# Optimization experiments

Hardware: AMD Instinct MI355X
Metric: run time of the kernel (lower is better)

Reference implementation:

```python
import jax, jax.numpy as jnp
import numpy as np

K = 15  # PSF kernel size


def conv3(x, w, b):
    # 3x3 conv, stride 1, padding 1, NCHW/OIHW
    y = jax.lax.conv_general_dilated(x, w, (1, 1), ((1, 1), (1, 1)),
                                     dimension_numbers=("NCHW", "OIHW", "NCHW"))
    return y + b[None, :, None, None]


def setup_inputs() -> dict:
    key = jax.random.key(0)
    ks = jax.random.split(key, 22)
    S = 0.05  # small init scale to keep activations / softmax logits sane
    p = lambda k, shape: (jax.random.normal(k, shape, jnp.float32) * S)
    return {
        "raw_image": jax.random.uniform(ks[0], (1, 4, 256, 256), jnp.float32),
        "aberration_features": jax.random.normal(ks[1], (1, 128, 256, 256), jnp.float32),
        # psf_predictor: 128->256->128->4*225
        "pw1": p(ks[2], (256, 128, 3, 3)), "pb1": p(ks[3], (256,)),
        "pw2": p(ks[4], (128, 256, 3, 3)), "pb2": p(ks[5], (128,)),
        "pw3": p(ks[6], (900, 128, 3, 3)), "pb3": p(ks[7], (900,)),
        # freq_corrector: 8->64->64->8
        "fw1": p(ks[8], (64, 8, 3, 3)),  "fb1": p(ks[9], (64,)),
        "fw2": p(ks[10], (64, 64, 3, 3)), "fb2": p(ks[11], (64,)),
        "fw3": p(ks[12], (8, 64, 3, 3)),  "fb3": p(ks[13], (8,)),
        # per-channel correctors (4 of them), stacked on leading dim: 1->16->16->1
        "cw1": p(ks[14], (4, 16, 1, 3, 3)),  "cb1": p(ks[15], (4, 16)),
        "cw2": p(ks[16], (4, 16, 16, 3, 3)), "cb2": p(ks[17], (4, 16)),
        "cw3": p(ks[18], (4, 1, 16, 3, 3)),  "cb3": p(ks[19], (4, 1)),
    }


def reference(raw_image, aberration_features,
              pw1, pb1, pw2, pb2, pw3, pb3,
              fw1, fb1, fw2, fb2, fw3, fb3,
              cw1, cb1, cw2, cb2, cw3, cb3):
    B, C, H, W = raw_image.shape
    # --- PSF prediction ---
    h = jax.nn.relu(conv3(aberration_features, pw1, pb1))
    h = jax.nn.relu(conv3(h, pw2, pb2))
    psf = conv3(h, pw3, pb3).reshape(B, C, K * K, H, W)
    psf = jax.nn.softmax(psf, axis=2)  # normalize over the K*K taps
    # --- spatially-varying deconv: unfold + weighted reduce ---
    pad = K // 2
    xp = jnp.pad(raw_image, ((0, 0), (0, 0), (pad, pad), (pad, pad)), mode="reflect")
    patches = jax.lax.conv_general_dilated_patches(
        xp, (K, K), (1, 1), "VALID", dimension_numbers=("NCHW", "OIHW", "NCHW"))
    patches = patches.reshape(B, C, K * K, H, W)  # channel-major like F.unfold
    corrected = jnp.sum(patches * psf, axis=2)  # [B,C,H,W]
    # --- frequency-domain correction ---
    fft = jnp.fft.rfft2(corrected, norm="ortho")  # [B,C,H,W//2+1] complex
    fri = jnp.concatenate([fft.real, fft.imag], axis=1)  # [B,2C,...]
    g = jax.nn.relu(conv3(fri, fw1, fb1))
    g = jax.nn.relu(conv3(g, fw2, fb2))
    g = conv3(g, fw3, fb3)
    cf = jax.lax.complex(g[:, :C], g[:, C:])
    corrected = corrected + jnp.fft.irfft2(cf, s=(H, W), norm="ortho")
    # --- per-channel refinement (4 small distinct conv stacks) ---
    outs = []
    for i in range(C):
        ch = corrected[:, i:i + 1]
        ch = jax.nn.relu(conv3(ch, cw1[i], cb1[i]))
        ch = jax.nn.relu(conv3(ch, cw2[i], cb2[i]))
        ch = conv3(ch, cw3[i], cb3[i])
        outs.append(ch)
    corrected = jnp.concatenate(outs, axis=1)
    return jnp.clip(raw_image + corrected, 0.0, 1.0)
```

## Files before the change

### kernel.cpp

```cpp
#include <hip/hip_runtime.h>
#include <hip/hip_bf16.h>
#include <math.h>

#define PI_F 3.14159265358979323846f
#define PERM4(s) ((((s)&3)) + 8*(((s)>>2)&1) + 4*((s)>>3))

typedef short bfrag __attribute__((ext_vector_type(8)));
typedef float f32x4 __attribute__((ext_vector_type(4)));
typedef float f32x16 __attribute__((ext_vector_type(16)));
typedef unsigned short us8 __attribute__((ext_vector_type(8)));

__device__ inline unsigned bf16rne(float x) {
    unsigned u = __builtin_bit_cast(unsigned, x);
    return (u + 0x7fffu + ((u >> 16) & 1u)) >> 16;
}
__device__ inline unsigned packbf2(float a, float b) {
    return bf16rne(a) | (bf16rne(b) << 16);
}
__device__ inline float bf2f(unsigned short u) {
    return __builtin_bit_cast(float, (unsigned)u << 16);
}
__device__ inline void glds16(const unsigned short* g, unsigned char* l) {
    __builtin_amdgcn_global_load_lds(
        (const __attribute__((address_space(1))) unsigned int*)g,
        (__attribute__((address_space(3))) unsigned int*)l, 16, 0, 0);
}

template<bool RELU, int CT, bool SM>
__global__ __launch_bounds__(256, (CT == 2) ? 4 : 5) void conv_v9(
    const unsigned short* __restrict__ inb, const short* __restrict__ wp,
    const float* __restrict__ bias, unsigned short* __restrict__ ob,
    int C32, int Cout, int COT, int CBmax,
    const float* __restrict__ rawc, float* __restrict__ corr)
{
    int bid = blockIdx.x;
    bid = (bid & 7) * 128 + (bid >> 3);
    const int y  = bid >> 2;
    const int x0 = (bid & 3) << 6;
    const int t  = threadIdx.x;
    const int l  = t & 63;
    const int col = l & 31, kh = l >> 5;
    const int wv = t >> 6;
    const int ctg0 = wv * CT;

    __shared__ __align__(16) unsigned char sB[2][13824];

    f32x16 acc[CT][2];
#pragma unroll
    for (int ct = 0; ct < CT; ++ct)
#pragma unroll
        for (int n = 0; n < 2; ++n)
#pragma unroll
            for (int i = 0; i < 16; ++i) acc[ct][n][i] = 0.f;

    int ba3[3];
#pragma unroll
    for (int dx = 0; dx < 3; ++dx) {
        int px = col + 3 + dx;
        ba3[dx] = px * 64 + ((kh ^ ((px >> 1) & 3)) << 4);
    }

    int srcoff[4];
    bool vmask[4];
#pragma unroll
    for (int i = 0; i < 4; ++i) {
        int q = i * 256 + t;
        bool qv = q < 864;
        int row = q / 288;  if (row > 2) row = 2;
        int qr = q - row * 288;
        int px = qr >> 2, j = qr & 3;
        int u = j ^ ((px >> 1) & 3);
        int gx = x0 - 4 + px;
        int gy = y - 1 + row;
        vmask[i] = qv && ((unsigned)gx < 256u) && ((unsigned)gy < 256u);
        srcoff[i] = (((u >> 1) * 256 + gy) * 256 + gx) * 16 + (u & 1) * 8;
    }

    auto STAGE = [&](int c32, unsigned char* bufb) {
        const int coff = c32 * 2097152;
#pragma unroll
        for (int i = 0; i < 4; ++i)
            if (vmask[i])
                glds16(inb + (srcoff[i] + coff), bufb + (i << 12) + (wv << 10));
    };

    for (int i = t; i < 1728; i += 256)
        *(uint4*)(&sB[0][0] + i * 16) = make_uint4(0, 0, 0, 0);
    __syncthreads();

    const bfrag* wA = (const bfrag*)wp;
    const int tstr = C32 * 2 * COT * 64;

    auto LOAD_AF = [&](bfrag (&af)[3][CT], int abase, int dy) {
#pragma unroll
        for (int dx = 0; dx < 3; ++dx)
#pragma unroll
            for (int ct = 0; ct < CT; ++ct)
                af[dx][ct] = wA[abase + ct * 64 + (size_t)(dy * 3 + dx) * tstr];
    };
    auto MFMA_DY = [&](const bfrag (&af)[3][CT], const unsigned char* rp, int csx) {
#pragma unroll
        for (int dx = 0; dx < 3; ++dx) {
            const int ba = ba3[dx] ^ csx;
            bfrag b0 = *(const bfrag*)(rp + ba);
            bfrag b1 = *(const bfrag*)(rp + ba + 2048);
#pragma unroll
            for (int ct = 0; ct < CT; ++ct) {
                acc[ct][0] = __builtin_amdgcn_mfma_f32_32x32x16_bf16(af[dx][ct], b0, acc[ct][0], 0, 0, 0);
                acc[ct][1] = __builtin_amdgcn_mfma_f32_32x32x16_bf16(af[dx][ct], b1, acc[ct][1], 0, 0, 0);
            }
        }
    };

    STAGE(0, sB[0]);
    __syncthreads();
    for (int c32 = 0; c32 < C32; ++c32) {
        const unsigned char* bufp = sB[c32 & 1];
        const int ab0 = (c32 * 2 * COT + ctg0) * 64 + l;
        const int ab1 = ((c32 * 2 + 1) * COT + ctg0) * 64 + l;
        bfrag af0[3][CT];
        LOAD_AF(af0, ab0, 0);
        if (c32 + 1 < C32) STAGE(c32 + 1, sB[(c32 + 1) & 1]);
        MFMA_DY(af0, bufp, 0);
#pragma unroll
        for (int dy = 1; dy < 3; ++dy) {
            bfrag af[3][CT];
            LOAD_AF(af, ab0, dy);
            MFMA_DY(af, bufp + dy * 4608, 0);
        }
#pragma unroll
        for (int dy = 0; dy < 3; ++dy) {
            bfrag af[3][CT];
            LOAD_AF(af, ab1, dy);
            MFMA_DY(af, bufp + dy * 4608, 32);
        }
        __syncthreads();
    }

    if (SM) {
        float* sRaw  = (float*)&sB[0][0];
        float* sBias = (float*)&sB[0][4800];
        float* red   = (float*)&sB[1][0];
        for (int i = t; i < 1200; i += 256) {
            int r = i / 80, xx = i - r * 80;
            int gy = y + r - 7;
            gy = gy < 0 ? -gy : (gy > 255 ? 510 - gy : gy);
            int gx = x0 + xx - 7;
            gx = gx < 0 ? -gx : (gx > 255 ? 510 - gx : gx);
            sRaw[i] = rawc[gy * 256 + gx];
        }
        if (t < 225) sBias[t] = bias[t];
        __syncthreads();

        float pm[2], ps[2], pa[2];
#pragma unroll
        for (int n = 0; n < 2; ++n) {
            float m = -1e30f, s = 0.f, a = 0.f;
            const int xb = col + n * 32;
#pragma unroll
            for (int ct = 0; ct < CT; ++ct) {
                const f32x16 A = acc[ct][n];
#pragma unroll
                for (int rh = 0; rh < 2; ++rh) {
                    int cb = (ctg0 + ct) * 2 + rh;
#pragma unroll
                    for (int j = 0; j < 8; ++j) {
                        int co = cb * 16 + (j & 3) + 8 * (j >> 2) + 4 * kh;
                        if (co < 225) {
                            float lv = A[rh * 8 + j] + sBias[co];
                            int ty = co / 15, tx = co - ty * 15;
                            float pv = sRaw[ty * 80 + xb + tx];
                            if (lv > m + 4.f) { float rs = __expf(m - lv); s *= rs; a *= rs; m = lv; }
                            float e = __expf(lv - m);
                            s += e; a += e * pv;
                        }
                    }
                }
            }
            pm[n] = m; ps[n] = s; pa[n] = a;
        }
        const int g = wv * 2 + kh;
#pragma unroll
        for (int n = 0; n < 2; ++n) {
            int px = col + n * 32;
            red[(px * 8 + g) * 3 + 0] = pm[n];
            red[(px * 8 + g) * 3 + 1] = ps[n];
            red[(px * 8 + g) * 3 + 2] = pa[n];
        }
        __syncthreads();
        if (t < 64) {
            float m = red[(t * 8) * 3], s = red[(t * 8) * 3 + 1], a = red[(t * 8) * 3 + 2];
#pragma unroll
            for (int gg = 1; gg < 8; ++gg) {
                float mg = red[(t * 8 + gg) * 3], sg = red[(t * 8 + gg) * 3 + 1], ag = red[(t * 8 + gg) * 3 + 2];
                float M = fmaxf(m, mg);
                float s0 = __expf(m - M), s1 = __expf(mg - M);
                s = s * s0 + sg * s1;
                a = a * s0 + ag * s1;
                m = M;
            }
            corr[y * 256 + x0 + t] = a / s;
        }
    } else {
#pragma unroll
        for (int ct = 0; ct < CT; ++ct) {
            const int ctg = ctg0 + ct;
#pragma unroll
            for (int n = 0; n < 2; ++n) {
                const int xx = x0 + col + n * 32;
                const f32x16 A = acc[ct][n];
#pragma unroll
                for (int rh = 0; rh < 2; ++rh) {
                    int cb = ctg * 2 + rh;
                    if (cb >= CBmax) continue;
                    unsigned wd[4];
#pragma unroll
                    for (int jp = 0; jp < 4; ++jp) {
                        float vv[2];
#pragma unroll
                        for (int e = 0; e < 2; ++e) {
                            int j = jp * 2 + e;
                            int co = cb * 16 + (j & 3) + 8 * (j >> 2) + 4 * kh;
                            float bv = (co < Cout) ? bias[co] : 0.f;
                            float v = A[rh * 8 + j] + bv;
                            if (RELU) v = fmaxf(v, 0.f);
                            vv[e] = v;
                        }
                        wd[jp] = packbf2(vv[0], vv[1]);
                    }
                    *(uint4*)(ob + ((((size_t)cb << 8) + y) * 256 + xx) * 16 + (kh << 3)) =
                        make_uint4(wd[0], wd[1], wd[2], wd[3]);
                }
            }
        }
    }
}

template<bool RELU, bool OUT_BF16, int CT>
__global__ __launch_bounds__(256, 3) void conv_v4(
    const unsigned short* __restrict__ inb, const short* __restrict__ wp,
    const float* __restrict__ bias, void* __restrict__ outv,
    int C32, int Cout, int COT, int W, int RSg, int CBmax)
{
    const int tilesx = (W + 127) >> 7;
    const int y  = blockIdx.x / tilesx;
    const int x0 = (blockIdx.x % tilesx) << 7;
    const int t  = threadIdx.x;
    const int l  = t & 63;
    const int col = l & 31, kh = l >> 5;
    const int wv = t >> 6;
    const int wct = wv & 1, wpt = wv >> 1;
    const int ctg0 = (blockIdx.y * 2 + wct) * CT;

    __shared__ __align__(16) unsigned char sB[26112];

    f32x16 acc[CT][2];
#pragma unroll
    for (int ct = 0; ct < CT; ++ct)
#pragma unroll
        for (int n = 0; n < 2; ++n)
#pragma unroll
            for (int i = 0; i < 16; ++i) acc[ct][n][i] = 0.f;

    int ba3[3];
#pragma unroll
    for (int dx = 0; dx < 3; ++dx) {
        int px = wpt * 64 + col + 3 + dx;
        ba3[dx] = px * 64 + ((kh ^ ((px >> 1) & 3)) << 4);
    }

    const int pxm = (t & 127) + 4, thalf = t >> 7;
    const int gxm = x0 + (t & 127);
    const bool gxok = gxm < W;
    const int offm_e = pxm * 64 + ((thalf ^ ((pxm >> 1) & 3)) << 4);
    const int hr = t >> 5, hj = t & 31, hg = hj >> 3, hp = hj & 7;
    const int hslot = hp + ((hp >> 2) << 7);
    const int hgx = x0 - 4 + hslot;
    const int hoff = hr * 8704 + hslot * 64 + ((hg ^ ((hslot >> 1) & 3)) << 4);
    const int hgy = y + hr - 1;
    const bool hok = (t < 96) && ((unsigned)hgy < 256u) && ((unsigned)hgx < (unsigned)W);

    auto STAGE = [&](int c32) {
        const int cb0 = c32 << 1;
#pragma unroll
        for (int k = 0; k < 6; ++k) {
            const int r = k >> 1;
            const int cb = cb0 + (k & 1);
            const int gy = y + r - 1;
            uint4 v = make_uint4(0, 0, 0, 0);
            if (gxok && (unsigned)gy < 256u)
                v = *(const uint4*)(inb + ((((size_t)cb << 8) + gy) * RSg + gxm) * 16 + (thalf << 3));
            *(uint4*)(sB + r * 8704 + (offm_e ^ ((k & 1) << 5))) = v;
        }
        if (t < 96) {
            uint4 v = make_uint4(0, 0, 0, 0);
            if (hok) v = *(const uint4*)(inb + ((((size_t)(cb0 + (hg >> 1)) << 8) + hgy) * RSg + hgx) * 16 + ((hg & 1) << 3));
            *(uint4*)(sB + hoff) = v;
        }
    };

    const bfrag* wA = (const bfrag*)wp;
    const int tstr = C32 * 2 * COT * 64;

    STAGE(0);
    __syncthreads();
    for (int c32 = 0; c32 < C32; ++c32) {
#pragma unroll 1
        for (int cs = 0; cs < 2; ++cs) {
            const int abase = ((c32 * 2 + cs) * COT + ctg0) * 64 + l;
            const int csx = cs << 5;
#pragma unroll
            for (int dy = 0; dy < 3; ++dy) {
                bfrag af[3][CT];
#pragma unroll
                for (int dx = 0; dx < 3; ++dx)
#pragma unroll
                    for (int ct = 0; ct < CT; ++ct)
                        af[dx][ct] = wA[abase + ct * 64 + (size_t)(dy * 3 + dx) * tstr];
                const unsigned char* rp = sB + dy * 8704;
#pragma unroll
                for (int dx = 0; dx < 3; ++dx) {
                    const int ba = ba3[dx] ^ csx;
                    bfrag b0 = *(const bfrag*)(rp + ba);
                    bfrag b1 = *(const bfrag*)(rp + ba + 2048);
#pragma unroll
                    for (int ct = 0; ct < CT; ++ct) {
                        acc[ct][0] = __builtin_amdgcn_mfma_f32_32x32x16_bf16(af[dx][ct], b0, acc[ct][0], 0, 0, 0);
                        acc[ct][1] = __builtin_amdgcn_mfma_f32_32x32x16_bf16(af[dx][ct], b1, acc[ct][1], 0, 0, 0);
                    }
                }
            }
        }
        __syncthreads();
        if (c32 + 1 < C32) { STAGE(c32 + 1); __syncthreads(); }
    }

    const int xBase = x0 + wpt * 64 + col;
#pragma unroll
    for (int ct = 0; ct < CT; ++ct) {
        const int ctg = ctg0 + ct;
#pragma unroll
        for (int n = 0; n < 2; ++n) {
            int xx = xBase + n * 32;
            if (xx >= W) continue;
            const f32x16 A = acc[ct][n];
            if (OUT_BF16) {
                unsigned short* ob = (unsigned short*)outv;
#pragma unroll
                for (int rh = 0; rh < 2; ++rh) {
                    int cb = ctg * 2 + rh;
                    if (cb >= CBmax) continue;
                    unsigned wd[4];
#pragma unroll
                    for (int jp = 0; jp < 4; ++jp) {
                        float vv[2];
#pragma unroll
                        for (int e = 0; e < 2; ++e) {
                            int j = jp * 2 + e;
                            int co = cb * 16 + (j & 3) + 8 * (j >> 2) + 4 * kh;
                            float bv = (co < Cout) ? bias[co] : 0.f;
                            float v = A[rh * 8 + j] + bv;
                            if (RELU) v = fmaxf(v, 0.f);
                            vv[e] = v;
                        }
                        wd[jp] = packbf2(vv[0], vv[1]);
                    }
                    *(uint4*)(ob + ((((size_t)cb << 8) + y) * RSg + xx) * 16 + (kh << 3)) =
                        make_uint4(wd[0], wd[1], wd[2], wd[3]);
                }
            } else {
                float* of = (float*)outv;
#pragma unroll
                for (int reg = 0; reg < 16; ++reg) {
                    int co = ctg * 32 + (reg & 3) + 8 * (reg >> 2) + 4 * kh;
                    if (co < Cout) {
                        float v = A[reg] + bias[co];
                        if (RELU) v = fmaxf(v, 0.f);
                        of[(((size_t)co << 8) + y) * RSg + xx] = v;
                    }
                }
            }
        }
    }
}

__global__ __launch_bounds__(256) void repack_wA(
    const float* __restrict__ w, unsigned short* __restrict__ o,
    int Cin, int C32, int Cout, int COT)
{
    int total = 9 * C32 * 2 * COT * 512;
    for (int i = blockIdx.x * 256 + threadIdx.x; i < total; i += gridDim.x * 256) {
        int j = i & 7;
        int l = (i >> 3) & 63;
        int rest = i >> 9;
        int ct = rest % COT; rest /= COT;
        int cs = rest & 1; rest >>= 1;
        int c32 = rest % C32;
        int tap = rest / C32;
        int co = ct * 32 + (l & 31);
        int s = ((l >> 5) << 3) + j;
        int ci = c32 * 32 + cs * 16 + PERM4(s);
        float v = (co < Cout && ci < Cin) ? w[((size_t)co * Cin + ci) * 9 + tap] : 0.f;
        o[i] = (unsigned short)bf16rne(v);
    }
}

__global__ __launch_bounds__(256) void cvt_blocked(
    const float* __restrict__ src, unsigned short* __restrict__ dst, int C)
{
    int cb = blockIdx.x >> 8;
    int y  = blockIdx.x & 255;
    int x  = threadIdx.x;
    unsigned wd[8];
#pragma unroll
    for (int q = 0; q < 8; ++q) {
        float v[2];
#pragma unroll
        for (int e = 0; e < 2; ++e) {
            int s = q * 2 + e;
            int ci = (cb << 4) + PERM4(s);
            v[e] = (ci < C) ? src[((size_t)ci * 256 + y) * 256 + x] : 0.f;
        }
        wd[q] = packbf2(v[0], v[1]);
    }
    unsigned short* dp = dst + (((size_t)cb << 16) + (y << 8) + x) * 16;
    *(uint4*)dp = make_uint4(wd[0], wd[1], wd[2], wd[3]);
    *(uint4*)(dp + 8) = make_uint4(wd[4], wd[5], wd[6], wd[7]);
}

__global__ __launch_bounds__(256) void repack_wr2(
    const float* __restrict__ cw2, unsigned short* __restrict__ o)
{
    int i = blockIdx.x * 256 + threadIdx.x;
    if (i >= 10240) return;
    int k = i & 31, rest = i >> 5;
    int co = rest & 15;
    int kt = (rest >> 4) % 5;
    int ch = rest / 80;
    int tap = 2 * kt + (k >= 16 ? 1 : 0), ci = k & 15;
    float v = 0.f;
    if (tap < 9) v = cw2[(((size_t)ch * 16 + co) * 16 + ci) * 9 + tap];
    o[i] = (unsigned short)bf16rne(v);
}

__global__ __launch_bounds__(256) void refine1_kernel(
    const float* __restrict__ corrected, const float* __restrict__ cw1,
    const float* __restrict__ cb1, unsigned short* __restrict__ h1b)
{
    const int c = blockIdx.x >> 8;
    const int y = blockIdx.x & 255;
    const int t = threadIdx.x;
    __shared__ float sIn[3][258];
    __shared__ float sW[144];
    __shared__ float sBv[16];
    if (t < 144) sW[t] = cw1[c * 144 + t];
    if (t >= 144 && t < 160) sBv[t - 144] = cb1[c * 16 + (t - 144)];
    for (int i = t; i < 774; i += 256) {
        int r = i / 258, xx = i % 258;
        int gy = y + r - 1, gx = xx - 1;
        sIn[r][xx] = ((unsigned)gy < 256u && (unsigned)gx < 256u)
                   ? corrected[((size_t)c * 256 + gy) * 256 + gx] : 0.f;
    }
    __syncthreads();
    float a[9];
#pragma unroll
    for (int dy = 0; dy < 3; ++dy)
#pragma unroll
        for (int dx = 0; dx < 3; ++dx) a[dy * 3 + dx] = sIn[dy][t + dx];
    unsigned short ov[16];
#pragma unroll
    for (int co = 0; co < 16; ++co) {
        float acc = sBv[co];
#pragma unroll
        for (int tap = 0; tap < 9; ++tap) acc += a[tap] * sW[co * 9 + tap];
        acc = fmaxf(acc, 0.f);
        ov[co] = (unsigned short)bf16rne(acc);
    }
    unsigned short* op = h1b + ((((size_t)c * 256 + y) * 256 + t) << 4);
    *(uint4*)op = *(uint4*)ov;
    *(uint4*)(op + 8) = *(uint4*)(ov + 8);
}

__global__ __launch_bounds__(256) void refine2_mfma(
    const unsigned short* __restrict__ h1b, const unsigned short* __restrict__ wr2,
    const float* __restrict__ cb2, unsigned short* __restrict__ h2b)
{
    const int c = blockIdx.x >> 8;
    const int y = blockIdx.x & 255;
    const int t = threadIdx.x;
    const int l15 = t & 15, lg = (t >> 4) & 3, wv = t >> 6;

    __shared__ __align__(16) unsigned char sA[3 * 258 * 32];

    for (int i = t; i < 1548; i += 256) {
        int r = i / 516, u = i % 516;
        int px = u >> 1, half = u & 1;
        int gy = y + r - 1, gx = px - 1;
        uint4 v = make_uint4(0, 0, 0, 0);
        if ((unsigned)gy < 256u && (unsigned)gx < 256u)
            v = *(const uint4*)(h1b + ((((size_t)c * 256 + gy) * 256 + gx) << 4) + (half << 3));
        *(uint4*)(sA + r * 8256 + px * 32 + ((half ^ ((px >> 2) & 1)) << 4)) = v;
    }
    __syncthreads();

    f32x4 acc[4];
#pragma unroll
    for (int n = 0; n < 4; ++n) acc[n] = (f32x4){0.f, 0.f, 0.f, 0.f};
    const bfrag* wf = (const bfrag*)(wr2 + (size_t)c * 2560);
    const int strip = wv * 64;
#pragma unroll
    for (int kt = 0; kt < 5; ++kt) {
        bfrag a = wf[(kt * 16 + l15) * 4 + lg];
        int tap1 = 2 * kt + 1; if (tap1 > 8) tap1 = 8;
        int tap = (lg < 2) ? (2 * kt) : tap1;
        int dy = tap / 3, dx = tap % 3;
#pragma unroll
        for (int n = 0; n < 4; ++n) {
            int pxs = strip + n * 16 + l15 + dx;
            bfrag b = *(const bfrag*)(sA + dy * 8256 + pxs * 32 +
                                      (((lg & 1) ^ ((pxs >> 2) & 1)) << 4));
            acc[n] = __builtin_amdgcn_mfma_f32_16x16x32_bf16(a, b, acc[n], 0, 0, 0);
        }
    }

#pragma unroll
    for (int n = 0; n < 4; ++n) {
        int px = strip + n * 16 + l15;
        unsigned short ov[4];
#pragma unroll
        for (int r = 0; r < 4; ++r) {
            int co = lg * 4 + r;
            float v = acc[n][r] + cb2[c * 16 + co];
            v = fmaxf(v, 0.f);
            ov[r] = (unsigned short)bf16rne(v);
        }
        *(ushort4*)(h2b + ((((size_t)c * 256 + y) * 256 + px) << 4) + lg * 4) = *(ushort4*)ov;
    }
}

__global__ __launch_bounds__(256) void refine3_kernel(
    const unsigned short* __restrict__ h2b, const float* __restrict__ cw3,
    const float* __restrict__ cb3, const float* __restrict__ raw,
    float* __restrict__ out)
{
    const int c = blockIdx.x >> 8;
    const int y = blockIdx.x & 255;
    const int t = threadIdx.x;
    __shared__ __align__(16) unsigned char sA[3 * 258 * 32];
    __shared__ float sW[144];
    if (t < 144) sW[t] = cw3[c * 144 + t];
    for (int i = t; i < 1548; i += 256) {
        int r = i / 516, u = i % 516;
        int px = u >> 1, half = u & 1;
        int gy = y + r - 1, gx = px - 1;
        uint4 v = make_uint4(0, 0, 0, 0);
        if ((unsigned)gy < 256u && (unsigned)gx < 256u)
            v = *(const uint4*)(h2b + ((((size_t)c * 256 + gy) * 256 + gx) << 4) + (half << 3));
        *(uint4*)(sA + r * 8256 + px * 32 + ((half ^ ((px >> 2) & 1)) << 4)) = v;
    }
    __syncthreads();
    float acc = cb3[c];
#pragma unroll
    for (int tap = 0; tap < 9; ++tap) {
        int dy = tap / 3, dx = tap % 3;
        int px = t + dx;
        const unsigned char* p = sA + dy * 8256 + px * 32;
        int sw = ((px >> 2) & 1) << 4;
        us8 h0 = *(const us8*)(p + (sw ^ 0));
        us8 h1 = *(const us8*)(p + (sw ^ 16));
#pragma unroll
        for (int j = 0; j < 8; ++j) acc += bf2f(h0[j]) * sW[j * 9 + tap];
#pragma unroll
        for (int j = 0; j < 8; ++j) acc += bf2f(h1[j]) * sW[(8 + j) * 9 + tap];
    }
    size_t idx = ((size_t)c * 256 + y) * 256 + t;
    float v = raw[idx] + acc;
    out[idx] = fminf(fmaxf(v, 0.f), 1.f);
}

__global__ __launch_bounds__(256) void rdft_row_kernel(
    const float* __restrict__ x, float2* __restrict__ z)
{
    int cy = blockIdx.x;
    __shared__ float row[256];
    __shared__ float ct[256], st[256];
    int t = threadIdx.x;
    row[t] = x[cy * 256 + t];
    float a = (2.0f * PI_F / 256.0f) * (float)t;
    ct[t] = cosf(a);
    st[t] = sinf(a);
    __syncthreads();
    if (t < 129) {
        float re = 0.f, im = 0.f;
        int idx = 0;
        for (int n = 0; n < 256; ++n) {
            float v = row[n];
            re += v * ct[idx];
            im -= v * st[idx];
            idx = (idx + t) & 255;
        }
        z[cy * 129 + t] = make_float2(re, im);
    }
}

__global__ __launch_bounds__(256) void dft_col_fwd2(
    const float2* __restrict__ z, unsigned short* __restrict__ fri16)
{
    int c  = blockIdx.x >> 8;
    int k1 = blockIdx.x & 255;
    __shared__ float ct[256], st[256];
    int t = threadIdx.x;
    float a = (2.0f * PI_F / 256.0f) * (float)t;
    ct[t] = cosf(a);
    st[t] = sinf(a);
    __syncthreads();
    if (t < 129) {
        float re = 0.f, im = 0.f;
        int idx = 0;
        for (int n1 = 0; n1 < 256; ++n1) {
            float2 zv = z[(c * 256 + n1) * 129 + t];
            float cw = ct[idx], sw = st[idx];
            re += zv.x * cw + zv.y * sw;
            im += zv.y * cw - zv.x * sw;
            idx = (idx + k1) & 255;
        }
        const float sc = 1.0f / 256.0f;
        size_t base = ((size_t)k1 * 132 + t) * 16;
        fri16[base + c]     = (unsigned short)bf16rne(re * sc);
        fri16[base + 8 + c] = (unsigned short)bf16rne(im * sc);
    }
}

__global__ __launch_bounds__(256) void dft_col_inv_kernel(
    const float* __restrict__ g, float2* __restrict__ z)
{
    int c  = blockIdx.x >> 8;
    int n1 = blockIdx.x & 255;
    __shared__ float ct[256], st[256];
    int t = threadIdx.x;
    float a = (2.0f * PI_F / 256.0f) * (float)t;
    ct[t] = cosf(a);
    st[t] = sinf(a);
    __syncthreads();
    if (t < 129) {
        float re = 0.f, im = 0.f;
        int idx = 0;
        for (int k1 = 0; k1 < 256; ++k1) {
            float gr = g[((size_t)c * 256 + k1) * 132 + t];
            float gi = g[((size_t)(4 + c) * 256 + k1) * 132 + t];
            float cw = ct[idx], sw = st[idx];
            re += gr * cw - gi * sw;
            im += gi * cw + gr * sw;
            idx = (idx + n1) & 255;
        }
        z[(c * 256 + n1) * 129 + t] = make_float2(re, im);
    }
}

__global__ __launch_bounds__(256) void irdft_row_add_kernel(
    const float2* __restrict__ z, float* __restrict__ corrected)
{
    int c  = blockIdx.x >> 8;
    int n1 = blockIdx.x & 255;
    __shared__ float2 yrow[129];
    __shared__ float ct[256], st[256];
    int t = threadIdx.x;
    if (t < 129) yrow[t] = z[(c * 256 + n1) * 129 + t];
    float a = (2.0f * PI_F / 256.0f) * (float)t;
    ct[t] = cosf(a);
    st[t] = sinf(a);
    __syncthreads();
    float acc = yrow[0].x + ((t & 1) ? -yrow[128].x : yrow[128].x);
    int idx = t;
    for (int k = 1; k <= 127; ++k) {
        float2 yv = yrow[k];
        acc += 2.0f * (yv.x * ct[idx] - yv.y * st[idx]);
        idx = (idx + t) & 255;
    }
    corrected[c * 65536 + n1 * 256 + t] += acc * (1.0f / 256.0f);
}

extern "C" void kernel_launch(void* const* d_in, const int* in_sizes, int n_in,
                              void* d_out, int out_size, void* d_ws, size_t ws_size,
                              hipStream_t stream)
{
    const float* raw = (const float*)d_in[0];
    const float* ab  = (const float*)d_in[1];
    const float* pw1 = (const float*)d_in[2];  const float* pb1 = (const float*)d_in[3];
    const float* pw2 = (const float*)d_in[4];  const float* pb2 = (const float*)d_in[5];
    const float* pw3 = (const float*)d_in[6];  const float* pb3 = (const float*)d_in[7];
    const float* fw1 = (const float*)d_in[8];  const float* fb1 = (const float*)d_in[9];
    const float* fw2 = (const float*)d_in[10]; const float* fb2 = (const float*)d_in[11];
    const float* fw3 = (const float*)d_in[12]; const float* fb3 = (const float*)d_in[13];
    const float* cw1 = (const float*)d_in[14]; const float* cb1 = (const float*)d_in[15];
    const float* cw2 = (const float*)d_in[16]; const float* cb2 = (const float*)d_in[17];
    const float* cw3 = (const float*)d_in[18]; const float* cb3 = (const float*)d_in[19];
    float* out = (float*)d_out;

    char* B = (char*)d_ws;
    unsigned short* h1b     = (unsigned short*)(B);
    unsigned short* h2b     = (unsigned short*)(B + 33554432);
    unsigned short* h1r     = (unsigned short*)(B + 33554432);
    unsigned short* h2r     = (unsigned short*)(B + 41943040);
    float* corrected = (float*)(B + 50331648);
    float2* zbuf     = (float2*)(B + 51380224);
    unsigned short* fri16 = (unsigned short*)(B + 53493760);
    unsigned short* g1b   = (unsigned short*)(B + 55656448);
    unsigned short* g2b   = (unsigned short*)(B + 59981824);
    float* gf        = (float*)(B + 64307200);
    unsigned short* rw1  = (unsigned short*)(B + 65388544);
    unsigned short* rw2  = (unsigned short*)(B + 65978368);
    unsigned short* rw3  = (unsigned short*)(B + 66568192);
    unsigned short* rwf1 = (unsigned short*)(B + 68927488);
    unsigned short* rwf2 = (unsigned short*)(B + 68964352);
    unsigned short* rwf3 = (unsigned short*)(B + 69038080);
    unsigned short* wr2r = (unsigned short*)(B + 69111808);
    unsigned short* ab16 = (unsigned short*)(B + 69132288);

    dim3 blk(256);

    repack_wA<<<512, blk, 0, stream>>>(pw1, rw1, 128, 4, 256, 8);
    repack_wA<<<512, blk, 0, stream>>>(pw2, rw2, 256, 8, 128, 4);
    for (int c = 0; c < 4; ++c)
        repack_wA<<<512, blk, 0, stream>>>(
            pw3 + (size_t)c * 225 * 128 * 9, rw3 + (size_t)c * 294912, 128, 4, 225, 8);
    repack_wA<<<64, blk, 0, stream>>>(fw1, rwf1, 8, 1, 64, 2);
    repack_wA<<<128, blk, 0, stream>>>(fw2, rwf2, 64, 2, 64, 2);
    repack_wA<<<128, blk, 0, stream>>>(fw3, rwf3, 64, 2, 8, 2);
    repack_wr2<<<40, blk, 0, stream>>>(cw2, wr2r);
    cvt_blocked<<<2048, blk, 0, stream>>>(ab, ab16, 128);

    conv_v9<true, 2, false><<<1024, blk, 0, stream>>>(
        ab16, (const short*)rw1, pb1, h1b, 4, 256, 8, 16, nullptr, nullptr);
    conv_v9<true, 1, false><<<1024, blk, 0, stream>>>(
        h1b, (const short*)rw2, pb2, h2b, 8, 128, 4, 8, nullptr, nullptr);
    for (int c = 0; c < 4; ++c) {
        conv_v9<false, 2, true><<<1024, blk, 0, stream>>>(
            h2b, (const short*)(rw3 + (size_t)c * 294912), pb3 + c * 225, h1b,
            4, 225, 8, 15, raw + c * 65536, corrected + c * 65536);
    }
    rdft_row_kernel<<<1024, blk, 0, stream>>>(corrected, zbuf);
    hipMemsetAsync(fri16, 0, 2162688, stream);
    dft_col_fwd2<<<1024, blk, 0, stream>>>(zbuf, fri16);
    conv_v4<true, true, 1><<<dim3(512, 1), blk, 0, stream>>>(
        fri16, (const short*)rwf1, fb1, g1b, 1, 64, 2, 129, 132, 4);
    conv_v4<true, true, 1><<<dim3(512, 1), blk, 0, stream>>>(
        g1b, (const short*)rwf2, fb2, g2b, 2, 64, 2, 129, 132, 4);
    conv_v4<false, false, 1><<<dim3(512, 1), blk, 0, stream>>>(
        g2b, (const short*)rwf3, fb3, gf, 2, 8, 2, 129, 132, 0);
    dft_col_inv_kernel<<<1024, blk, 0, stream>>>(gf, zbuf);
    irdft_row_add_kernel<<<1024, blk, 0, stream>>>(zbuf, corrected);
    refine1_kernel<<<1024, blk, 0, stream>>>(corrected, cw1, cb1, h1r);
    refine2_mfma<<<1024, blk, 0, stream>>>(h1r, wr2r, cb2, h2r);
    refine3_kernel<<<1024, blk, 0, stream>>>(h2r, cw3, cb3, raw, out);
}
```

Baseline: 471.7 us.

## Double-buffer conv weight fragments across channel halves and simplify softmax reduction

```diff
diff --git a/kernel.cpp b/kernel.cpp
--- a/kernel.cpp
+++ b/kernel.cpp
@@ -27,7 +27,7 @@
 }
 
 template<bool RELU, int CT, bool SM>
-__global__ __launch_bounds__(256, (CT == 2) ? 4 : 5) void conv_v9(
+__global__ __launch_bounds__(256, (CT == 2) ? 4 : 5) void conv_v10(
     const unsigned short* __restrict__ inb, const short* __restrict__ wp,
     const float* __restrict__ bias, unsigned short* __restrict__ ob,
     int C32, int Cout, int COT, int CBmax,
@@ -91,55 +91,51 @@
     const bfrag* wA = (const bfrag*)wp;
     const int tstr = C32 * 2 * COT * 64;
 
-    auto LOAD_AF = [&](bfrag (&af)[3][CT], int abase, int dy) {
-#pragma unroll
-        for (int dx = 0; dx < 3; ++dx)
+    auto LOAD_CS = [&](bfrag (&af)[9][CT], int c32, int cs) {
+        const int abase = ((c32 * 2 + cs) * COT + ctg0) * 64 + l;
+#pragma unroll
+        for (int tap = 0; tap < 9; ++tap)
 #pragma unroll
             for (int ct = 0; ct < CT; ++ct)
-                af[dx][ct] = wA[abase + ct * 64 + (size_t)(dy * 3 + dx) * tstr];
+                af[tap][ct] = wA[abase + ct * 64 + (size_t)tap * tstr];
     };
-    auto MFMA_DY = [&](const bfrag (&af)[3][CT], const unsigned char* rp, int csx) {
-#pragma unroll
-        for (int dx = 0; dx < 3; ++dx) {
-            const int ba = ba3[dx] ^ csx;
-            bfrag b0 = *(const bfrag*)(rp + ba);
-            bfrag b1 = *(const bfrag*)(rp + ba + 2048);
-#pragma unroll
-            for (int ct = 0; ct < CT; ++ct) {
-                acc[ct][0] = __builtin_amdgcn_mfma_f32_32x32x16_bf16(af[dx][ct], b0, acc[ct][0], 0, 0, 0);
-                acc[ct][1] = __builtin_amdgcn_mfma_f32_32x32x16_bf16(af[dx][ct], b1, acc[ct][1], 0, 0, 0);
+    auto MFMA_CS = [&](const bfrag (&af)[9][CT], const unsigned char* bufp, int csx) {
+#pragma unroll
+        for (int dy = 0; dy < 3; ++dy) {
+            const unsigned char* rp = bufp + dy * 4608;
+#pragma unroll
+            for (int dx = 0; dx < 3; ++dx) {
+                const int ba = ba3[dx] ^ csx;
+                bfrag b0 = *(const bfrag*)(rp + ba);
+                bfrag b1 = *(const bfrag*)(rp + ba + 2048);
+#pragma unroll
+                for (int ct = 0; ct < CT; ++ct) {
+                    acc[ct][0] = __builtin_amdgcn_mfma_f32_32x32x16_bf16(af[dy * 3 + dx][ct], b0, acc[ct][0], 0, 0, 0);
+                    acc[ct][1] = __builtin_amdgcn_mfma_f32_32x32x16_bf16(af[dy * 3 + dx][ct], b1, acc[ct][1], 0, 0, 0);
+                }
             }
         }
     };
 
+    bfrag afA[9][CT], afB[9][CT];
     STAGE(0, sB[0]);
+    LOAD_CS(afA, 0, 0);
     __syncthreads();
     for (int c32 = 0; c32 < C32; ++c32) {
         const unsigned char* bufp = sB[c32 & 1];
-        const int ab0 = (c32 * 2 * COT + ctg0) * 64 + l;
-        const int ab1 = ((c32 * 2 + 1) * COT + ctg0) * 64 + l;
-        bfrag af0[3][CT];
-        LOAD_AF(af0, ab0, 0);
-        if (c32 + 1 < C32) STAGE(c32 + 1, sB[(c32 + 1) & 1]);
-        MFMA_DY(af0, bufp, 0);
-#pragma unroll
-        for (int dy = 1; dy < 3; ++dy) {
-            bfrag af[3][CT];
-            LOAD_AF(af, ab0, dy);
-            MFMA_DY(af, bufp + dy * 4608, 0);
-        }
-#pragma unroll
-        for (int dy = 0; dy < 3; ++dy) {
-            bfrag af[3][CT];
-            LOAD_AF(af, ab1, dy);
-            MFMA_DY(af, bufp + dy * 4608, 32);
-        }
+        const bool more = c32 + 1 < C32;
+        LOAD_CS(afB, c32, 1);
+        if (more) STAGE(c32 + 1, sB[(c32 + 1) & 1]);
+        MFMA_CS(afA, bufp, 0);
+        if (more) LOAD_CS(afA, c32 + 1, 0);
+        MFMA_CS(afB, bufp, 32);
         __syncthreads();
     }
 
     if (SM) {
         float* sRaw  = (float*)&sB[0][0];
         float* sBias = (float*)&sB[0][4800];
+        int*   sOff  = (int*)&sB[0][5700];
         float* red   = (float*)&sB[1][0];
         for (int i = t; i < 1200; i += 256) {
             int r = i / 80, xx = i - r * 80;
@@ -149,7 +145,10 @@
             gx = gx < 0 ? -gx : (gx > 255 ? 510 - gx : gx);
             sRaw[i] = rawc[gy * 256 + gx];
         }
-        if (t < 225) sBias[t] = bias[t];
+        if (t < 225) {
+            sBias[t] = bias[t];
+            sOff[t]  = t + 65 * (t / 15);
+        }
         __syncthreads();
 
         float pm[2], ps[2], pa[2];
@@ -168,8 +167,7 @@
                         int co = cb * 16 + (j & 3) + 8 * (j >> 2) + 4 * kh;
                         if (co < 225) {
                             float lv = A[rh * 8 + j] + sBias[co];
-                            int ty = co / 15, tx = co - ty * 15;
-                            float pv = sRaw[ty * 80 + xb + tx];
+                            float pv = sRaw[sOff[co] + xb];
                             if (lv > m + 4.f) { float rs = __expf(m - lv); s *= rs; a *= rs; m = lv; }
                             float e = __expf(lv - m);
                             s += e; a += e * pv;
@@ -177,22 +175,28 @@
                     }
                 }
             }
-            pm[n] = m; ps[n] = s; pa[n] = a;
-        }
-        const int g = wv * 2 + kh;
-#pragma unroll
-        for (int n = 0; n < 2; ++n) {
-            int px = col + n * 32;
-            red[(px * 8 + g) * 3 + 0] = pm[n];
-            red[(px * 8 + g) * 3 + 1] = ps[n];
-            red[(px * 8 + g) * 3 + 2] = pa[n];
+            float mo = __shfl_xor(m, 32), so = __shfl_xor(s, 32), ao = __shfl_xor(a, 32);
+            float M = fmaxf(m, mo);
+            float e0 = __expf(m - M), e1 = __expf(mo - M);
+            pm[n] = M;
+            ps[n] = s * e0 + so * e1;
+            pa[n] = a * e0 + ao * e1;
+        }
+        if (kh == 0) {
+#pragma unroll
+            for (int n = 0; n < 2; ++n) {
+                int px = col + n * 32;
+                red[(px * 4 + wv) * 3 + 0] = pm[n];
+                red[(px * 4 + wv) * 3 + 1] = ps[n];
+                red[(px * 4 + wv) * 3 + 2] = pa[n];
+            }
         }
         __syncthreads();
         if (t < 64) {
-            float m = red[(t * 8) * 3], s = red[(t * 8) * 3 + 1], a = red[(t * 8) * 3 + 2];
-#pragma unroll
-            for (int gg = 1; gg < 8; ++gg) {
-                float mg = red[(t * 8 + gg) * 3], sg = red[(t * 8 + gg) * 3 + 1], ag = red[(t * 8 + gg) * 3 + 2];
+            float m = red[(t * 4) * 3], s = red[(t * 4) * 3 + 1], a = red[(t * 4) * 3 + 2];
+#pragma unroll
+            for (int gg = 1; gg < 4; ++gg) {
+                float mg = red[(t * 4 + gg) * 3], sg = red[(t * 4 + gg) * 3 + 1], ag = red[(t * 4 + gg) * 3 + 2];
                 float M = fmaxf(m, mg);
                 float s0 = __expf(m - M), s1 = __expf(mg - M);
                 s = s * s0 + sg * s1;
@@ -730,12 +734,12 @@
     repack_wr2<<<40, blk, 0, stream>>>(cw2, wr2r);
     cvt_blocked<<<2048, blk, 0, stream>>>(ab, ab16, 128);
 
-    conv_v9<true, 2, false><<<1024, blk, 0, stream>>>(
+    conv_v10<true, 2, false><<<1024, blk, 0, stream>>>(
         ab16, (const short*)rw1, pb1, h1b, 4, 256, 8, 16, nullptr, nullptr);
-    conv_v9<true, 1, false><<<1024, blk, 0, stream>>>(
+    conv_v10<true, 1, false><<<1024, blk, 0, stream>>>(
         h1b, (const short*)rw2, pb2, h2b, 8, 128, 4, 8, nullptr, nullptr);
     for (int c = 0; c < 4; ++c) {
-        conv_v9<false, 2, true><<<1024, blk, 0, stream>>>(
+        conv_v10<false, 2, true><<<1024, blk, 0, stream>>>(
             h2b, (const short*)(rw3 + (size_t)c * 294912), pb3 + c * 225, h1b,
             4, 225, 8, 15, raw + c * 65536, corrected + c * 65536);
     }
```

New measurement: 1.096 ms. 132% more time.
